# Performance work log

Measured on AMD Instinct MI355X. Metric: run time of the kernel, lower is better.

Reference implementation:

```python
import jax, jax.numpy as jnp
import numpy as np
from jax import lax

DIM = 256
HEADS = 8
P = 4  # split_size (patch_size)
SCALE = (DIM // HEADS) ** -0.5  # note: scale uses full head_dim = dim//heads, per the torch code


def _win(t, p1, p2, h):
    # 'b (h d) (gx p1) (gy p2) -> (b gx gy) h (p1 p2) d'
    b, c, X, Y = t.shape
    d = c // h
    gx, gy = X // p1, Y // p2
    t = t.reshape(b, h, d, gx, p1, gy, p2).transpose(0, 3, 5, 1, 4, 6, 2)
    return t.reshape(b * gx * gy, h, p1 * p2, d)


def _unwin(v, b, gx, gy, h, p1, p2):
    # '(b gx gy) h (p1 p2) d -> b (h d) (gx p1) (gy p2)'
    d = v.shape[-1]
    v = v.reshape(b, gx, gy, h, p1, p2, d).transpose(0, 3, 6, 1, 4, 2, 5)
    return v.reshape(b, h * d, gx * p1, gy * p2)


def _conv(x, w, stride):
    return lax.conv_general_dilated(x, w, stride, 'VALID',
                                    dimension_numbers=('NCHW', 'OIHW', 'NCHW'))


def _attn_branch(q, k, v, lepe):
    # q: (G,h,Nq,d), k/lepe: (G,h,Nk,d), v: (G,h,Nq,d)
    attn = jax.nn.softmax((q * SCALE) @ jnp.swapaxes(k, -2, -1), axis=-1)  # (G,h,Nq,Nk)
    # torch does attn.transpose(-2,-1) @ v + lepe -> output indexed by key tokens
    return jnp.einsum('ghqk,ghqd->ghkd', attn, v) + lepe


def setup_inputs() -> dict:
    key = jax.random.key(0)
    ks = jax.random.split(key, 6)
    b, x, y = 16, 64, 64
    fmap = jax.random.normal(ks[0], (b, DIM, x, y), dtype=jnp.float32)
    W_qvh = jax.random.normal(ks[1], (DIM, DIM // 2, 2, 1), dtype=jnp.float32) * 0.02
    W_qvv = jax.random.normal(ks[2], (DIM, DIM // 2, 1, 2), dtype=jnp.float32) * 0.02
    W_k = jax.random.normal(ks[3], (DIM, DIM), dtype=jnp.float32) * 0.02
    W_lepe = jax.random.normal(ks[4], (DIM, DIM), dtype=jnp.float32) * 0.02
    W_proj = jax.random.normal(ks[5], (DIM, DIM), dtype=jnp.float32) * 0.02
    return {"fmap": fmap, "W_qvh": W_qvh, "W_qvv": W_qvv,
            "W_k": W_k, "W_lepe": W_lepe, "W_proj": W_proj}


def reference(fmap, W_qvh, W_qvv, W_k, W_lepe, W_proj):
    b, n, x, y = fmap.shape
    h, p = HEADS, P
    half = n // 2
    # strided qv projections (size=0 path)
    qv_h = _conv(fmap[:, :half], W_qvh, (2, 1))  # (b, n, x/2, y)
    qv_v = _conv(fmap[:, half:], W_qvv, (1, 2))  # (b, n, x, y/2)
    # 1x1 convs as channel matmuls
    k_all = jnp.einsum('bcxy,oc->boxy', fmap, W_k)
    lepe_all = jnp.einsum('bcxy,oc->boxy', fmap, W_lepe)

    # horizontal branch: strips of width p spanning full height
    q_h = _win(qv_h[:, :half], x // 2, p, h)     # (b*(y/p), h, (x/2)*p, d)
    v_h = _win(qv_h[:, half:], x // 2, p, h)
    k_h = _win(k_all[:, :half], x, p, h)         # (b*(y/p), h, x*p, d)
    lepe_h = _win(lepe_all[:, :half], x, p, h)
    out_h = _attn_branch(q_h, k_h, v_h, lepe_h)  # (b*(y/p), h, x*p, d)
    out_h = _unwin(out_h, b, 1, y // p, h, x, p)  # (b, n/2, x, y)

    # vertical branch: strips of height p spanning full width
    q_v = _win(qv_v[:, :half], p, y // 2, h)
    v_v = _win(qv_v[:, half:], p, y // 2, h)
    k_v = _win(k_all[:, half:], p, y, h)
    lepe_v = _win(lepe_all[:, half:], p, y, h)
    out_v = _attn_branch(q_v, k_v, v_v, lepe_v)
    out_v = _unwin(out_v, b, x // p, 1, h, p, y)  # (b, n/2, x, y)

    cat = jnp.concatenate([out_h, out_v], axis=1)  # (b, n, x, y)
    return fmap + jnp.einsum('bcxy,oc->boxy', cat, W_proj)
```

## Files before the change

kernel.cpp:

```cpp
#include <hip/hip_runtime.h>
#include <hip/hip_bf16.h>

#define SCALE 0.1767766952966369f

typedef unsigned short bfu;
typedef unsigned int u32;
typedef __attribute__((ext_vector_type(8))) short bf8v;
typedef __attribute__((ext_vector_type(4))) float f32x4;
typedef __attribute__((ext_vector_type(8))) unsigned short u16x8;
typedef __attribute__((ext_vector_type(4))) unsigned int u32x4;

__device__ __forceinline__ bfu f2b(float x) {
    __hip_bfloat16 h = __float2bfloat16(x);
    return *(bfu*)&h;
}
__device__ __forceinline__ float bu2f(bfu u) {
    return __uint_as_float(((unsigned int)u) << 16);
}
__device__ __forceinline__ u32 cvtpk(float lo, float hi) {
    u32 r;
    asm("v_cvt_pk_bf16_f32 %0, %1, %2" : "=v"(r) : "v"(lo), "v"(hi));
    return r;
}
__device__ __forceinline__ void gload16(const bfu* g, bfu* l) {
    __builtin_amdgcn_global_load_lds(
        (const __attribute__((address_space(1))) unsigned int*)g,
        (__attribute__((address_space(3))) unsigned int*)l, 16, 0, 0);
}

__global__ __launch_bounds__(256) void k_prep_f(const float* __restrict__ fmap,
                                                bfu* __restrict__ Fbf) {
    const int x = blockIdx.x, b = blockIdx.y;
    const int t = threadIdx.x;
    __shared__ float tile[64][69];
    for (int cc = 0; cc < 256; cc += 64) {
        #pragma unroll
        for (int i = 0; i < 4; ++i) {
            const int c = (t >> 4) + i * 16, y4 = (t & 15) * 4;
            const float4 v = *(const float4*)(fmap + (((size_t)b * 256 + cc + c) * 64 + x) * 64 + y4);
            tile[y4][c] = v.x; tile[y4 + 1][c] = v.y; tile[y4 + 2][c] = v.z; tile[y4 + 3][c] = v.w;
        }
        __syncthreads();
        const int y = t >> 2, cs = (t & 3) * 16;
        u16x8 o0, o1;
        #pragma unroll
        for (int j = 0; j < 8; ++j) { o0[j] = f2b(tile[y][cs + j]); o1[j] = f2b(tile[y][cs + 8 + j]); }
        bfu* dst = Fbf + (((size_t)b * 64 + x) * 64 + y) * 256 + cc + cs;
        *(u16x8*)dst = o0; *(u16x8*)(dst + 8) = o1;
        __syncthreads();
    }
}

__global__ __launch_bounds__(256) void k_prep_w(
    const float* __restrict__ Wk, const float* __restrict__ Wl,
    const float* __restrict__ Wh, const float* __restrict__ Wv,
    bfu* __restrict__ Wkl, bfu* __restrict__ Whr, bfu* __restrict__ Wvr) {
    const int i = blockIdx.x * 256 + threadIdx.x;
    {
        const int o = i >> 8;
        Wkl[i] = f2b((o < 256) ? Wk[i] : Wl[i - 65536]);
    }
    if (i < 65536) {
        const int o = i >> 8, r = i & 255, kh = r >> 7, c = r & 127;
        const int s = (o * 128 + c) * 2 + kh;
        Whr[i] = f2b(Wh[s]);
        Wvr[i] = f2b(Wv[s]);
    }
}

template<int MODE>
__global__ __launch_bounds__(256) void k_gemm(
    const bfu* __restrict__ Ab16, const float* __restrict__ Af32,
    const bfu* __restrict__ Bsrc,
    bfu* __restrict__ o_kall, bfu* __restrict__ o_lepe, bfu* __restrict__ o_qv,
    const float* __restrict__ resid, float* __restrict__ outf) {
    const int nt = blockIdx.x, mt = blockIdx.y, b = blockIdx.z;
    const int n0 = nt * 128, m0 = mt * 128;
    const int t = threadIdx.x, lane = t & 63;
    const int wave = t >> 6, wm = wave >> 1, wn = wave & 1;
    const int lq = lane >> 4, lr = lane & 15;
    __shared__ bfu Bs[128 * 256];
    const bfu* fb = Bsrc + (size_t)b * 1048576;

    {
        const int lrow = lane >> 5;
        const int c1 = lane & 31;
        #pragma unroll
        for (int i = 0; i < 16; ++i) {
            const int row = wave * 32 + i * 2 + lrow;
            const int cS = c1 ^ (row & 7);
            int so;
            if (MODE == 0 || MODE == 3) {
                so = (n0 + row) * 256 + cS * 8;
            } else if (MODE == 1) {
                const int n = n0 + row;
                const int xo = n >> 6, y = n & 63;
                so = ((2 * xo + (cS >> 4)) * 64 + y) * 256 + (cS & 15) * 8;
            } else {
                const int n = n0 + row;
                const int x = n >> 5, yo = n & 31;
                so = (x * 64 + 2 * yo + (cS >> 4)) * 256 + 128 + (cS & 15) * 8;
            }
            gload16(fb + so, Bs + (wave * 32 + i * 2) * 256);
        }
    }
    __syncthreads();

    f32x4 acc[4][4];
    #pragma unroll
    for (int mi = 0; mi < 4; ++mi)
        #pragma unroll
        for (int ni = 0; ni < 4; ++ni) {
            acc[mi][ni][0] = 0.f; acc[mi][ni][1] = 0.f; acc[mi][ni][2] = 0.f; acc[mi][ni][3] = 0.f;
        }

    #pragma unroll
    for (int k0 = 0; k0 < 8; ++k0) {
        bf8v af[4], bv[4];
        if (MODE == 3) {
            #pragma unroll
            for (int mi = 0; mi < 4; ++mi) {
                const float* ap = Af32 + (size_t)(m0 + wm * 64 + mi * 16 + lr) * 256 + k0 * 32 + lq * 8;
                const float4 u0 = *(const float4*)ap;
                const float4 u1 = *(const float4*)(ap + 4);
                bf8v a;
                a[0] = (short)f2b(u0.x); a[1] = (short)f2b(u0.y);
                a[2] = (short)f2b(u0.z); a[3] = (short)f2b(u0.w);
                a[4] = (short)f2b(u1.x); a[5] = (short)f2b(u1.y);
                a[6] = (short)f2b(u1.z); a[7] = (short)f2b(u1.w);
                af[mi] = a;
            }
        } else {
            #pragma unroll
            for (int mi = 0; mi < 4; ++mi)
                af[mi] = *(const bf8v*)(Ab16 + (size_t)(m0 + wm * 64 + mi * 16 + lr) * 256 + k0 * 32 + lq * 8);
        }
        #pragma unroll
        for (int ni = 0; ni < 4; ++ni) {
            const int row = wn * 64 + ni * 16 + lr;
            const int ck = (k0 * 4 + lq) ^ (row & 7);
            bv[ni] = *(const bf8v*)(Bs + row * 256 + ck * 8);
        }
        #pragma unroll
        for (int mi = 0; mi < 4; ++mi)
            #pragma unroll
            for (int ni = 0; ni < 4; ++ni)
                acc[mi][ni] = __builtin_amdgcn_mfma_f32_16x16x32_bf16(af[mi], bv[ni], acc[mi][ni], 0, 0, 0);
    }

    if (MODE == 0) {
        bfu* outp = (mt < 2) ? o_kall : o_lepe;
        const int chb = (mt & 1) * 128 + wm * 64;
        #pragma unroll
        for (int mi = 0; mi < 4; ++mi)
            #pragma unroll
            for (int ni = 0; ni < 4; ++ni) {
                const int ch = chb + mi * 16 + lq * 4;
                const int ng = n0 + wn * 64 + ni * 16 + lr;
                ushort4 pk;
                pk.x = f2b(acc[mi][ni][0]); pk.y = f2b(acc[mi][ni][1]);
                pk.z = f2b(acc[mi][ni][2]); pk.w = f2b(acc[mi][ni][3]);
                *(ushort4*)(outp + ((size_t)b * 4096 + ng) * 256 + ch) = pk;
            }
    } else if (MODE == 1 || MODE == 2) {
        #pragma unroll
        for (int mi = 0; mi < 4; ++mi)
            #pragma unroll
            for (int ni = 0; ni < 4; ++ni) {
                const int ch = m0 + wm * 64 + mi * 16 + lq * 4;
                const int ng = n0 + wn * 64 + ni * 16 + lr;
                ushort4 pk;
                pk.x = f2b(acc[mi][ni][0]); pk.y = f2b(acc[mi][ni][1]);
                pk.z = f2b(acc[mi][ni][2]); pk.w = f2b(acc[mi][ni][3]);
                *(ushort4*)(o_qv + ((size_t)b * 2048 + ng) * 256 + ch) = pk;
            }
    } else {
        #pragma unroll
        for (int mi = 0; mi < 4; ++mi)
            #pragma unroll
            for (int ni = 0; ni < 4; ++ni) {
                const int ng = n0 + wn * 64 + ni * 16 + lr;
                #pragma unroll
                for (int r = 0; r < 4; ++r) {
                    const int m = m0 + wm * 64 + mi * 16 + lq * 4 + r;
                    const size_t ad = ((size_t)b * 256 + m) * 4096 + ng;
                    outf[ad] = resid[ad] + acc[mi][ni][r];
                }
            }
    }
}

template<int BR>
__global__ __launch_bounds__(256) void k_attn(
    const bfu* __restrict__ Qv, const bfu* __restrict__ Kb,
    const bfu* __restrict__ Lp, bfu* __restrict__ cat) {
    const int bid = blockIdx.x;
    const int h = (bid >> 8) & 7;
    const int bg = bid & 255;
    const int b = bg >> 4, g = bg & 15;
    const int t = threadIdx.x, lane = t & 63, w = t >> 6;
    const int lr = lane & 15, lq = lane >> 4;
    const int chQ = h * 16, chV = 128 + h * 16;
    const int chO = (BR == 0) ? h * 16 : 128 + h * 16;
    const bfu* Qb = Qv + (size_t)b * 2048 * 256;
    const bfu* Kg = Kb + (size_t)b * 4096 * 256 + chO;
    const bfu* Lg = Lp + (size_t)b * 4096 * 256 + chO;
    bfu* Cg = cat + (size_t)b * 4096 * 256 + chO;

    __shared__ float psum[2][256];

    bf8v kf[4];
    #pragma unroll
    for (int ct = 0; ct < 4; ++ct) {
        const int ktok = (4 * w + ct) * 16 + lr;
        const int sp = (BR == 0) ? ((ktok >> 2) * 64 + g * 4 + (ktok & 3))
                                 : ((g * 4 + (ktok >> 6)) * 64 + (ktok & 63));
        if (lq < 2) kf[ct] = *(const bf8v*)(Kg + (size_t)sp * 256 + lq * 8);
        else        kf[ct] = bf8v{0, 0, 0, 0, 0, 0, 0, 0};
    }

    f32x4 oacc[4];
    #pragma unroll
    for (int ct = 0; ct < 4; ++ct) { oacc[ct][0] = 0.f; oacc[ct][1] = 0.f; oacc[ct][2] = 0.f; oacc[ct][3] = 0.f; }

    for (int gq = 0; gq < 2; ++gq) {
        bf8v qf[4];
        #pragma unroll
        for (int qt = 0; qt < 4; ++qt) {
            const int qtok = gq * 64 + qt * 16 + lr;
            const int sp = (BR == 0) ? ((qtok >> 2) * 64 + g * 4 + (qtok & 3))
                                     : ((g * 4 + (qtok >> 5)) * 32 + (qtok & 31));
            if (lq < 2) qf[qt] = *(const bf8v*)(Qb + (size_t)sp * 256 + chQ + lq * 8);
            else        qf[qt] = bf8v{0, 0, 0, 0, 0, 0, 0, 0};
        }
        bf8v vf[2];
        #pragma unroll
        for (int c = 0; c < 2; ++c) {
            #pragma unroll
            for (int j = 0; j < 8; ++j) {
                const int qtok = gq * 64 + c * 32 + lq * 8 + j;
                const int sp = (BR == 0) ? ((qtok >> 2) * 64 + g * 4 + (qtok & 3))
                                         : ((g * 4 + (qtok >> 5)) * 32 + (qtok & 31));
                vf[c][j] = (short)Qb[(size_t)sp * 256 + chV + lr];
            }
        }

        f32x4 acc[4][4];
        #pragma unroll
        for (int qt = 0; qt < 4; ++qt)
            #pragma unroll
            for (int ct = 0; ct < 4; ++ct) {
                acc[qt][ct][0] = 0.f; acc[qt][ct][1] = 0.f; acc[qt][ct][2] = 0.f; acc[qt][ct][3] = 0.f;
            }
        #pragma unroll
        for (int qt = 0; qt < 4; ++qt)
            #pragma unroll
            for (int ct = 0; ct < 4; ++ct)
                acc[qt][ct] = __builtin_amdgcn_mfma_f32_16x16x32_bf16(qf[qt], kf[ct], acc[qt][ct], 0, 0, 0);

        #pragma unroll
        for (int qt = 0; qt < 4; ++qt)
            #pragma unroll
            for (int ct = 0; ct < 4; ++ct)
                #pragma unroll
                for (int r = 0; r < 4; ++r)
                    acc[qt][ct][r] = __expf(acc[qt][ct][r] * SCALE);

        float rr[4][4];
        #pragma unroll
        for (int qt = 0; qt < 4; ++qt)
            #pragma unroll
            for (int r = 0; r < 4; ++r)
                rr[qt][r] = (acc[qt][0][r] + acc[qt][1][r]) + (acc[qt][2][r] + acc[qt][3][r]);
        #pragma unroll
        for (int s = 1; s <= 8; s <<= 1)
            #pragma unroll
            for (int qt = 0; qt < 4; ++qt)
                #pragma unroll
                for (int r = 0; r < 4; ++r)
                    rr[qt][r] += __shfl_xor(rr[qt][r], s);
        if (lr == 0) {
            #pragma unroll
            for (int qt = 0; qt < 4; ++qt)
                #pragma unroll
                for (int r = 0; r < 4; ++r)
                    psum[gq][w * 64 + qt * 16 + lq * 4 + r] = rr[qt][r];
        }
        __syncthreads();
        float inv[4][4];
        #pragma unroll
        for (int qt = 0; qt < 4; ++qt)
            #pragma unroll
            for (int r = 0; r < 4; ++r) {
                const int qi = qt * 16 + lq * 4 + r;
                inv[qt][r] = 1.0f / ((psum[gq][qi] + psum[gq][64 + qi]) +
                                     (psum[gq][128 + qi] + psum[gq][192 + qi]));
            }

        u32 pk[4][4][2];
        #pragma unroll
        for (int qt = 0; qt < 4; ++qt)
            #pragma unroll
            for (int ct = 0; ct < 4; ++ct) {
                pk[qt][ct][0] = cvtpk(acc[qt][ct][0] * inv[qt][0], acc[qt][ct][1] * inv[qt][1]);
                pk[qt][ct][1] = cvtpk(acc[qt][ct][2] * inv[qt][2], acc[qt][ct][3] * inv[qt][3]);
            }

        const int base = ((lane >> 4) & 1) * 32 + (lane & 15);
        const bool hi = (lq >= 2);
        #pragma unroll
        for (int c = 0; c < 2; ++c) {
            #pragma unroll
            for (int ct = 0; ct < 4; ++ct) {
                const u32 a0 = (u32)__shfl((int)pk[2 * c][ct][0], base);
                const u32 a1 = (u32)__shfl((int)pk[2 * c][ct][1], base);
                const u32 a2 = (u32)__shfl((int)pk[2 * c][ct][0], base + 16);
                const u32 a3 = (u32)__shfl((int)pk[2 * c][ct][1], base + 16);
                const u32 b0 = (u32)__shfl((int)pk[2 * c + 1][ct][0], base);
                const u32 b1 = (u32)__shfl((int)pk[2 * c + 1][ct][1], base);
                const u32 b2 = (u32)__shfl((int)pk[2 * c + 1][ct][0], base + 16);
                const u32 b3 = (u32)__shfl((int)pk[2 * c + 1][ct][1], base + 16);
                u32x4 wd;
                wd[0] = hi ? b0 : a0; wd[1] = hi ? b1 : a1;
                wd[2] = hi ? b2 : a2; wd[3] = hi ? b3 : a3;
                const bf8v pf = __builtin_bit_cast(bf8v, wd);
                oacc[ct] = __builtin_amdgcn_mfma_f32_16x16x32_bf16(vf[c], pf, oacc[ct], 0, 0, 0);
            }
        }
    }

    #pragma unroll
    for (int ct = 0; ct < 4; ++ct) {
        const int ktok = (4 * w + ct) * 16 + lr;
        const int sp = (BR == 0) ? ((ktok >> 2) * 64 + g * 4 + (ktok & 3))
                                 : ((g * 4 + (ktok >> 6)) * 64 + (ktok & 63));
        const size_t off = (size_t)sp * 256 + lq * 4;
        const ushort4 l4 = *(const ushort4*)(Lg + off);
        ushort4 o;
        o.x = f2b(oacc[ct][0] + bu2f(l4.x));
        o.y = f2b(oacc[ct][1] + bu2f(l4.y));
        o.z = f2b(oacc[ct][2] + bu2f(l4.z));
        o.w = f2b(oacc[ct][3] + bu2f(l4.w));
        *(ushort4*)(Cg + off) = o;
    }
}

extern "C" void kernel_launch(void* const* d_in, const int* in_sizes, int n_in,
                              void* d_out, int out_size, void* d_ws, size_t ws_size,
                              hipStream_t stream) {
    const float* fmap = (const float*)d_in[0];
    const float* Wqvh = (const float*)d_in[1];
    const float* Wqvv = (const float*)d_in[2];
    const float* Wk   = (const float*)d_in[3];
    const float* Wl   = (const float*)d_in[4];
    const float* Wp   = (const float*)d_in[5];
    float* out = (float*)d_out;
    char* ws = (char*)d_ws;

    bfu* Fbf   = (bfu*)(ws);
    bfu* cat   = Fbf;
    bfu* k_all = (bfu*)(ws + 33554432);
    bfu* lepe  = (bfu*)(ws + 67108864);
    bfu* qvh   = (bfu*)(ws + 100663296);
    bfu* qvv   = (bfu*)(ws + 117440512);

    bfu* Wkl = (bfu*)d_out;
    bfu* Whr = (bfu*)((char*)d_out + 262144);
    bfu* Wvr = (bfu*)((char*)d_out + 393216);

    k_prep_f<<<dim3(64, 16), 256, 0, stream>>>(fmap, Fbf);
    k_prep_w<<<dim3(512), 256, 0, stream>>>(Wk, Wl, Wqvh, Wqvv, Wkl, Whr, Wvr);
    k_gemm<0><<<dim3(32, 4, 16), 256, 0, stream>>>(Wkl, nullptr, Fbf, k_all, lepe, nullptr, nullptr, nullptr);
    k_gemm<1><<<dim3(16, 2, 16), 256, 0, stream>>>(Whr, nullptr, Fbf, nullptr, nullptr, qvh, nullptr, nullptr);
    k_gemm<2><<<dim3(16, 2, 16), 256, 0, stream>>>(Wvr, nullptr, Fbf, nullptr, nullptr, qvv, nullptr, nullptr);
    k_attn<0><<<dim3(2048), 256, 0, stream>>>(qvh, k_all, lepe, cat);
    k_attn<1><<<dim3(2048), 256, 0, stream>>>(qvv, k_all, lepe, cat);
    k_gemm<3><<<dim3(32, 2, 16), 256, 0, stream>>>(nullptr, Wp, cat, nullptr, nullptr, nullptr, fmap, out);
}
```

Baseline: 259.0 us.

## Fuse k/lepe/qv projection GEMMs into one kernel sharing a staged fmap tile

Replaces the three separate projection GEMM launches (k/lepe, horizontal qv, vertical qv) with one kernel. Each block loads a 128-token fmap tile into shared memory once and reuses it for all four 128-channel k/lepe outputs and both strided qv convolutions. The output projection kernel likewise loops over both output-channel halves with one staged cat tile. This removes repeated global loads of the activation tile and extra launches. In exchange the grid shrinks from thousands of blocks to 512 per kernel, each running several times more sequential work, which lowers parallelism on a large GPU.

```diff
diff --git a/kernel.cpp b/kernel.cpp
--- a/kernel.cpp
+++ b/kernel.cpp
@@ -68,59 +68,195 @@
     }
 }
 
-template<int MODE>
-__global__ __launch_bounds__(256) void k_gemm(
-    const bfu* __restrict__ Ab16, const float* __restrict__ Af32,
-    const bfu* __restrict__ Bsrc,
-    bfu* __restrict__ o_kall, bfu* __restrict__ o_lepe, bfu* __restrict__ o_qv,
-    const float* __restrict__ resid, float* __restrict__ outf) {
-    const int nt = blockIdx.x, mt = blockIdx.y, b = blockIdx.z;
-    const int n0 = nt * 128, m0 = mt * 128;
-    const int t = threadIdx.x, lane = t & 63;
-    const int wave = t >> 6, wm = wave >> 1, wn = wave & 1;
+__global__ __launch_bounds__(256) void k_fused(
+    const bfu* __restrict__ Wkl, const bfu* __restrict__ Whr,
+    const bfu* __restrict__ Wvr, const bfu* __restrict__ Fbf,
+    bfu* __restrict__ o_kall, bfu* __restrict__ o_lepe,
+    bfu* __restrict__ o_qvh, bfu* __restrict__ o_qvv) {
+    const int tt = blockIdx.x, b = blockIdx.y;
+    const int tid = threadIdx.x, lane = tid & 63, wave = tid >> 6;
     const int lq = lane >> 4, lr = lane & 15;
     __shared__ bfu Bs[128 * 256];
-    const bfu* fb = Bsrc + (size_t)b * 1048576;
+    const bfu* src = Fbf + ((size_t)b * 4096 + tt * 128) * 256;
 
     {
-        const int lrow = lane >> 5;
-        const int c1 = lane & 31;
+        const int lrow = lane >> 5, c1 = lane & 31;
         #pragma unroll
         for (int i = 0; i < 16; ++i) {
             const int row = wave * 32 + i * 2 + lrow;
             const int cS = c1 ^ (row & 7);
-            int so;
-            if (MODE == 0 || MODE == 3) {
-                so = (n0 + row) * 256 + cS * 8;
-            } else if (MODE == 1) {
-                const int n = n0 + row;
-                const int xo = n >> 6, y = n & 63;
-                so = ((2 * xo + (cS >> 4)) * 64 + y) * 256 + (cS & 15) * 8;
-            } else {
-                const int n = n0 + row;
-                const int x = n >> 5, yo = n & 31;
-                so = (x * 64 + 2 * yo + (cS >> 4)) * 256 + 128 + (cS & 15) * 8;
-            }
-            gload16(fb + so, Bs + (wave * 32 + i * 2) * 256);
+            gload16(src + row * 256 + cS * 8, Bs + (wave * 32 + i * 2) * 256);
         }
     }
     __syncthreads();
 
-    f32x4 acc[4][4];
-    #pragma unroll
-    for (int mi = 0; mi < 4; ++mi)
-        #pragma unroll
-        for (int ni = 0; ni < 4; ++ni) {
-            acc[mi][ni][0] = 0.f; acc[mi][ni][1] = 0.f; acc[mi][ni][2] = 0.f; acc[mi][ni][3] = 0.f;
-        }
-
-    #pragma unroll
-    for (int k0 = 0; k0 < 8; ++k0) {
-        bf8v af[4], bv[4];
-        if (MODE == 3) {
+    const int wm = wave >> 1, wn = wave & 1;
+    for (int r = 0; r < 4; ++r) {
+        f32x4 acc[4][4];
+        #pragma unroll
+        for (int mi = 0; mi < 4; ++mi)
+            #pragma unroll
+            for (int ni = 0; ni < 4; ++ni) {
+                acc[mi][ni][0] = 0.f; acc[mi][ni][1] = 0.f;
+                acc[mi][ni][2] = 0.f; acc[mi][ni][3] = 0.f;
+            }
+        #pragma unroll
+        for (int k0 = 0; k0 < 8; ++k0) {
+            bf8v af[4], bv[4];
+            #pragma unroll
+            for (int mi = 0; mi < 4; ++mi)
+                af[mi] = *(const bf8v*)(Wkl + (size_t)(r * 128 + wm * 64 + mi * 16 + lr) * 256 + k0 * 32 + lq * 8);
+            #pragma unroll
+            for (int ni = 0; ni < 4; ++ni) {
+                const int row = wn * 64 + ni * 16 + lr;
+                const int ck = (k0 * 4 + lq) ^ (row & 7);
+                bv[ni] = *(const bf8v*)(Bs + row * 256 + ck * 8);
+            }
+            #pragma unroll
+            for (int mi = 0; mi < 4; ++mi)
+                #pragma unroll
+                for (int ni = 0; ni < 4; ++ni)
+                    acc[mi][ni] = __builtin_amdgcn_mfma_f32_16x16x32_bf16(af[mi], bv[ni], acc[mi][ni], 0, 0, 0);
+        }
+        bfu* outp = (r < 2) ? o_kall : o_lepe;
+        const int chb = (r & 1) * 128 + wm * 64;
+        #pragma unroll
+        for (int mi = 0; mi < 4; ++mi)
+            #pragma unroll
+            for (int ni = 0; ni < 4; ++ni) {
+                const int ch = chb + mi * 16 + lq * 4;
+                const int ng = tt * 128 + wn * 64 + ni * 16 + lr;
+                ushort4 pk;
+                pk.x = f2b(acc[mi][ni][0]); pk.y = f2b(acc[mi][ni][1]);
+                pk.z = f2b(acc[mi][ni][2]); pk.w = f2b(acc[mi][ni][3]);
+                *(ushort4*)(outp + ((size_t)b * 4096 + ng) * 256 + ch) = pk;
+            }
+    }
+
+    {
+        f32x4 acc[4][4];
+        #pragma unroll
+        for (int mi = 0; mi < 4; ++mi)
+            #pragma unroll
+            for (int ni = 0; ni < 4; ++ni) {
+                acc[mi][ni][0] = 0.f; acc[mi][ni][1] = 0.f;
+                acc[mi][ni][2] = 0.f; acc[mi][ni][3] = 0.f;
+            }
+        #pragma unroll
+        for (int k0 = 0; k0 < 8; ++k0) {
+            bf8v af[4], bv[4];
+            #pragma unroll
+            for (int mi = 0; mi < 4; ++mi)
+                af[mi] = *(const bf8v*)(Whr + (size_t)(wave * 64 + mi * 16 + lr) * 256 + k0 * 32 + lq * 8);
+            #pragma unroll
+            for (int ni = 0; ni < 4; ++ni) {
+                const int n = ni * 16 + lr;
+                const int row = ((k0 >= 4) ? 64 : 0) + n;
+                const int c = (k0 & 3) * 4 + lq;
+                const int ck = c ^ (row & 7);
+                bv[ni] = *(const bf8v*)(Bs + row * 256 + ck * 8);
+            }
+            #pragma unroll
+            for (int mi = 0; mi < 4; ++mi)
+                #pragma unroll
+                for (int ni = 0; ni < 4; ++ni)
+                    acc[mi][ni] = __builtin_amdgcn_mfma_f32_16x16x32_bf16(af[mi], bv[ni], acc[mi][ni], 0, 0, 0);
+        }
+        #pragma unroll
+        for (int mi = 0; mi < 4; ++mi)
+            #pragma unroll
+            for (int ni = 0; ni < 4; ++ni) {
+                const int ch = wave * 64 + mi * 16 + lq * 4;
+                const int ng = tt * 64 + ni * 16 + lr;
+                ushort4 pk;
+                pk.x = f2b(acc[mi][ni][0]); pk.y = f2b(acc[mi][ni][1]);
+                pk.z = f2b(acc[mi][ni][2]); pk.w = f2b(acc[mi][ni][3]);
+                *(ushort4*)(o_qvh + ((size_t)b * 2048 + ng) * 256 + ch) = pk;
+            }
+    }
+
+    {
+        f32x4 acc[4][4];
+        #pragma unroll
+        for (int mi = 0; mi < 4; ++mi)
+            #pragma unroll
+            for (int ni = 0; ni < 4; ++ni) {
+                acc[mi][ni][0] = 0.f; acc[mi][ni][1] = 0.f;
+                acc[mi][ni][2] = 0.f; acc[mi][ni][3] = 0.f;
+            }
+        #pragma unroll
+        for (int k0 = 0; k0 < 8; ++k0) {
+            bf8v af[4], bv[4];
+            #pragma unroll
+            for (int mi = 0; mi < 4; ++mi)
+                af[mi] = *(const bf8v*)(Wvr + (size_t)(wave * 64 + mi * 16 + lr) * 256 + k0 * 32 + lq * 8);
+            #pragma unroll
+            for (int ni = 0; ni < 4; ++ni) {
+                const int n = ni * 16 + lr;
+                const int xl = n >> 5, yo = n & 31;
+                const int row = xl * 64 + 2 * yo + ((k0 >= 4) ? 1 : 0);
+                const int c = 16 + (k0 & 3) * 4 + lq;
+                const int ck = c ^ (row & 7);
+                bv[ni] = *(const bf8v*)(Bs + row * 256 + ck * 8);
+            }
+            #pragma unroll
+            for (int mi = 0; mi < 4; ++mi)
+                #pragma unroll
+                for (int ni = 0; ni < 4; ++ni)
+                    acc[mi][ni] = __builtin_amdgcn_mfma_f32_16x16x32_bf16(af[mi], bv[ni], acc[mi][ni], 0, 0, 0);
+        }
+        #pragma unroll
+        for (int mi = 0; mi < 4; ++mi)
+            #pragma unroll
+            for (int ni = 0; ni < 4; ++ni) {
+                const int n = ni * 16 + lr;
+                const int ch = wave * 64 + mi * 16 + lq * 4;
+                const int ng = tt * 64 + n;
+                ushort4 pk;
+                pk.x = f2b(acc[mi][ni][0]); pk.y = f2b(acc[mi][ni][1]);
+                pk.z = f2b(acc[mi][ni][2]); pk.w = f2b(acc[mi][ni][3]);
+                *(ushort4*)(o_qvv + ((size_t)b * 2048 + ng) * 256 + ch) = pk;
+            }
+    }
+}
+
+__global__ __launch_bounds__(256) void k_proj(
+    const float* __restrict__ Wp, const bfu* __restrict__ cat,
+    const float* __restrict__ resid, float* __restrict__ outf) {
+    const int nt = blockIdx.x, b = blockIdx.y;
+    const int n0 = nt * 128;
+    const int tid = threadIdx.x, lane = tid & 63, wave = tid >> 6;
+    const int wm = wave >> 1, wn = wave & 1;
+    const int lq = lane >> 4, lr = lane & 15;
+    __shared__ bfu Bs[128 * 256];
+    const bfu* src = cat + ((size_t)b * 4096 + n0) * 256;
+
+    {
+        const int lrow = lane >> 5, c1 = lane & 31;
+        #pragma unroll
+        for (int i = 0; i < 16; ++i) {
+            const int row = wave * 32 + i * 2 + lrow;
+            const int cS = c1 ^ (row & 7);
+            gload16(src + row * 256 + cS * 8, Bs + (wave * 32 + i * 2) * 256);
+        }
+    }
+    __syncthreads();
+
+    for (int r = 0; r < 2; ++r) {
+        f32x4 acc[4][4];
+        #pragma unroll
+        for (int mi = 0; mi < 4; ++mi)
+            #pragma unroll
+            for (int ni = 0; ni < 4; ++ni) {
+                acc[mi][ni][0] = 0.f; acc[mi][ni][1] = 0.f;
+                acc[mi][ni][2] = 0.f; acc[mi][ni][3] = 0.f;
+            }
+        #pragma unroll
+        for (int k0 = 0; k0 < 8; ++k0) {
+            bf8v af[4], bv[4];
             #pragma unroll
             for (int mi = 0; mi < 4; ++mi) {
-                const float* ap = Af32 + (size_t)(m0 + wm * 64 + mi * 16 + lr) * 256 + k0 * 32 + lq * 8;
+                const float* ap = Wp + (size_t)(r * 128 + wm * 64 + mi * 16 + lr) * 256 + k0 * 32 + lq * 8;
                 const float4 u0 = *(const float4*)ap;
                 const float4 u1 = *(const float4*)(ap + 4);
                 bf8v a;
@@ -130,61 +266,28 @@
                 a[6] = (short)f2b(u1.z); a[7] = (short)f2b(u1.w);
                 af[mi] = a;
             }
-        } else {
-            #pragma unroll
-            for (int mi = 0; mi < 4; ++mi)
-                af[mi] = *(const bf8v*)(Ab16 + (size_t)(m0 + wm * 64 + mi * 16 + lr) * 256 + k0 * 32 + lq * 8);
-        }
-        #pragma unroll
-        for (int ni = 0; ni < 4; ++ni) {
-            const int row = wn * 64 + ni * 16 + lr;
-            const int ck = (k0 * 4 + lq) ^ (row & 7);
-            bv[ni] = *(const bf8v*)(Bs + row * 256 + ck * 8);
-        }
-        #pragma unroll
-        for (int mi = 0; mi < 4; ++mi)
-            #pragma unroll
-            for (int ni = 0; ni < 4; ++ni)
-                acc[mi][ni] = __builtin_amdgcn_mfma_f32_16x16x32_bf16(af[mi], bv[ni], acc[mi][ni], 0, 0, 0);
-    }
-
-    if (MODE == 0) {
-        bfu* outp = (mt < 2) ? o_kall : o_lepe;
-        const int chb = (mt & 1) * 128 + wm * 64;
-        #pragma unroll
-        for (int mi = 0; mi < 4; ++mi)
-            #pragma unroll
-            for (int ni = 0; ni < 4; ++ni) {
-                const int ch = chb + mi * 16 + lq * 4;
+            #pragma unroll
+            for (int ni = 0; ni < 4; ++ni) {
+                const int row = wn * 64 + ni * 16 + lr;
+                const int ck = (k0 * 4 + lq) ^ (row & 7);
+                bv[ni] = *(const bf8v*)(Bs + row * 256 + ck * 8);
+            }
+            #pragma unroll
+            for (int mi = 0; mi < 4; ++mi)
+                #pragma unroll
+                for (int ni = 0; ni < 4; ++ni)
+                    acc[mi][ni] = __builtin_amdgcn_mfma_f32_16x16x32_bf16(af[mi], bv[ni], acc[mi][ni], 0, 0, 0);
+        }
+        #pragma unroll
+        for (int mi = 0; mi < 4; ++mi)
+            #pragma unroll
+            for (int ni = 0; ni < 4; ++ni) {
                 const int ng = n0 + wn * 64 + ni * 16 + lr;
-                ushort4 pk;
-                pk.x = f2b(acc[mi][ni][0]); pk.y = f2b(acc[mi][ni][1]);
-                pk.z = f2b(acc[mi][ni][2]); pk.w = f2b(acc[mi][ni][3]);
-                *(ushort4*)(outp + ((size_t)b * 4096 + ng) * 256 + ch) = pk;
-            }
-    } else if (MODE == 1 || MODE == 2) {
-        #pragma unroll
-        for (int mi = 0; mi < 4; ++mi)
-            #pragma unroll
-            for (int ni = 0; ni < 4; ++ni) {
-                const int ch = m0 + wm * 64 + mi * 16 + lq * 4;
-                const int ng = n0 + wn * 64 + ni * 16 + lr;
-                ushort4 pk;
-                pk.x = f2b(acc[mi][ni][0]); pk.y = f2b(acc[mi][ni][1]);
-                pk.z = f2b(acc[mi][ni][2]); pk.w = f2b(acc[mi][ni][3]);
-                *(ushort4*)(o_qv + ((size_t)b * 2048 + ng) * 256 + ch) = pk;
-            }
-    } else {
-        #pragma unroll
-        for (int mi = 0; mi < 4; ++mi)
-            #pragma unroll
-            for (int ni = 0; ni < 4; ++ni) {
-                const int ng = n0 + wn * 64 + ni * 16 + lr;
-                #pragma unroll
-                for (int r = 0; r < 4; ++r) {
-                    const int m = m0 + wm * 64 + mi * 16 + lq * 4 + r;
+                #pragma unroll
+                for (int rr = 0; rr < 4; ++rr) {
+                    const int m = r * 128 + wm * 64 + mi * 16 + lq * 4 + rr;
                     const size_t ad = ((size_t)b * 256 + m) * 4096 + ng;
-                    outf[ad] = resid[ad] + acc[mi][ni][r];
+                    outf[ad] = resid[ad] + acc[mi][ni][rr];
                 }
             }
     }
@@ -370,10 +473,8 @@
 
     k_prep_f<<<dim3(64, 16), 256, 0, stream>>>(fmap, Fbf);
     k_prep_w<<<dim3(512), 256, 0, stream>>>(Wk, Wl, Wqvh, Wqvv, Wkl, Whr, Wvr);
-    k_gemm<0><<<dim3(32, 4, 16), 256, 0, stream>>>(Wkl, nullptr, Fbf, k_all, lepe, nullptr, nullptr, nullptr);
-    k_gemm<1><<<dim3(16, 2, 16), 256, 0, stream>>>(Whr, nullptr, Fbf, nullptr, nullptr, qvh, nullptr, nullptr);
-    k_gemm<2><<<dim3(16, 2, 16), 256, 0, stream>>>(Wvr, nullptr, Fbf, nullptr, nullptr, qvv, nullptr, nullptr);
+    k_fused<<<dim3(32, 16), 256, 0, stream>>>(Wkl, Whr, Wvr, Fbf, k_all, lepe, qvh, qvv);
     k_attn<0><<<dim3(2048), 256, 0, stream>>>(qvh, k_all, lepe, cat);
     k_attn<1><<<dim3(2048), 256, 0, stream>>>(qvv, k_all, lepe, cat);
-    k_gemm<3><<<dim3(32, 2, 16), 256, 0, stream>>>(nullptr, Wp, cat, nullptr, nullptr, nullptr, fmap, out);
-}
+    k_proj<<<dim3(32, 16), 256, 0, stream>>>(Wp, cat, fmap, out);
+}
```

Result: slower. 299.6 us (+15.7%).
